# Optimization experiments

Measured on AMD Instinct MI355X. Metric: run time of the kernel, lower is better.

The kernel has to match this reference:

```python
import jax, jax.numpy as jnp
import numpy as np

TOTAL = 409600   # flattened number of (id, rating) pairs across the batch
BATCH = 4096     # number of ragged segments (samples)
VOCAB = 1000000  # sum(field_dims)
DIM = 64         # embed_dim


def setup_inputs() -> dict:
    key = jax.random.key(0)
    k1, k2, k3, k4 = jax.random.split(key, 4)
    ids = jax.random.randint(k1, (TOTAL,), 0, VOCAB, dtype=jnp.int32)
    ratings = jax.random.uniform(k2, (TOTAL,), dtype=jnp.float32)
    segment_ids = jnp.sort(jax.random.randint(k3, (TOTAL,), 0, BATCH, dtype=jnp.int32))
    # Embedding table (xavier_uniform in the original; scale is irrelevant for correctness)
    table = jax.random.normal(k4, (VOCAB, DIM), dtype=jnp.float32) * 0.01
    return {"ids": ids, "ratings": ratings, "segment_ids": segment_ids, "table": table}


def reference(ids, ratings, segment_ids, table):
    # gather rows, scale by ratings, segment-sum over ragged per-sample groups
    emb = table[ids] * ratings[:, None]                      # [TOTAL, DIM]
    out = jax.ops.segment_sum(emb, segment_ids, num_segments=BATCH)  # [BATCH, DIM]
    return out
```

## Files before the change

kernel.cpp:

```cpp
#include <hip/hip_runtime.h>


#define TOTAL 409600
#define BATCH 4096
#define DIM   64
#define WAVES_PER_BLOCK 4

__global__ __launch_bounds__(256) void features_embedding_kernel(
    const int*   __restrict__ ids,
    const float* __restrict__ ratings,
    const int*   __restrict__ seg,
    const float* __restrict__ table,
    float*       __restrict__ out)
{
    const int wave = threadIdx.x >> 6;
    const int lane = threadIdx.x & 63;
    const int b    = blockIdx.x * WAVES_PER_BLOCK + wave;
    if (b >= BATCH) return;

    int lo = 0, hi = TOTAL;
    while (lo < hi) {
        int mid = (lo + hi) >> 1;
        if (seg[mid] < b) lo = mid + 1; else hi = mid;
    }
    int start = lo;
    hi = TOTAL;
    while (lo < hi) {
        int mid = (lo + hi) >> 1;
        if (seg[mid] < b + 1) lo = mid + 1; else hi = mid;
    }
    int end = lo;

    start = __builtin_amdgcn_readfirstlane(start);
    end   = __builtin_amdgcn_readfirstlane(end);

    float acc = 0.0f;
    int r = start;
    constexpr int U = 8;
    for (; r + U <= end; r += U) {
        int   id[U];
        float rt[U];
        #pragma unroll
        for (int u = 0; u < U; ++u) {
            id[u] = ids[r + u];
            rt[u] = ratings[r + u];
        }
        float v[U];
        #pragma unroll
        for (int u = 0; u < U; ++u)
            v[u] = table[(size_t)id[u] * DIM + lane];
        #pragma unroll
        for (int u = 0; u < U; ++u)
            acc = fmaf(v[u], rt[u], acc);
    }
    for (; r < end; ++r)
        acc = fmaf(table[(size_t)ids[r] * DIM + lane], ratings[r], acc);

    out[(size_t)b * DIM + lane] = acc;
}

extern "C" void kernel_launch(void* const* d_in, const int* in_sizes, int n_in,
                              void* d_out, int out_size, void* d_ws, size_t ws_size,
                              hipStream_t stream) {
    const int*   ids     = (const int*)  d_in[0];
    const float* ratings = (const float*)d_in[1];
    const int*   seg     = (const int*)  d_in[2];
    const float* table   = (const float*)d_in[3];
    float*       out     = (float*)      d_out;

    dim3 grid(BATCH / WAVES_PER_BLOCK);
    dim3 block(256);
    features_embedding_kernel<<<grid, block, 0, stream>>>(ids, ratings, seg, table, out);
}
```

Measured before the change: 326.5 us.

## Precompute segment offsets and gather rows with float4 across lane groups

Adds a pre-pass kernel that writes segment start offsets into the workspace, replacing the per-wave binary searches over the segment array. The main kernel now splits each wave into four 16-lane groups, and each group loads a whole 256-byte row as float4s, so four rows are in flight per wave instruction. A cross-group shuffle reduction follows before the store. The cost is an extra kernel launch and fewer independent rows per lane in the unrolled loop (4 instead of 8).

New measurement: 316.7 us. 3.0% less time.

```diff
diff --git a/kernel.cpp b/kernel.cpp
--- a/kernel.cpp
+++ b/kernel.cpp
@@ -4,59 +4,84 @@
 #define TOTAL 409600
 #define BATCH 4096
 #define DIM   64
-#define WAVES_PER_BLOCK 4
 
-__global__ __launch_bounds__(256) void features_embedding_kernel(
+__global__ __launch_bounds__(256) void seg_offsets_kernel(
+    const int* __restrict__ seg, int* __restrict__ offsets)
+{
+    int i = blockIdx.x * blockDim.x + threadIdx.x;
+    if (i >= TOTAL) return;
+    int cur  = seg[i];
+    int prev = (i == 0) ? -1 : seg[i - 1];
+    for (int b = prev + 1; b <= cur; ++b) offsets[b] = i;
+    if (i == TOTAL - 1) {
+        for (int b = cur + 1; b <= BATCH; ++b) offsets[b] = TOTAL;
+    }
+}
+
+__global__ __launch_bounds__(256) void embed_bag_kernel(
     const int*   __restrict__ ids,
     const float* __restrict__ ratings,
-    const int*   __restrict__ seg,
+    const int*   __restrict__ offsets,
     const float* __restrict__ table,
     float*       __restrict__ out)
 {
     const int wave = threadIdx.x >> 6;
     const int lane = threadIdx.x & 63;
-    const int b    = blockIdx.x * WAVES_PER_BLOCK + wave;
-    if (b >= BATCH) return;
+    const int b    = blockIdx.x * 4 + wave;
+    const int grp  = lane >> 4;
+    const int col  = lane & 15;
 
-    int lo = 0, hi = TOTAL;
-    while (lo < hi) {
-        int mid = (lo + hi) >> 1;
-        if (seg[mid] < b) lo = mid + 1; else hi = mid;
-    }
-    int start = lo;
-    hi = TOTAL;
-    while (lo < hi) {
-        int mid = (lo + hi) >> 1;
-        if (seg[mid] < b + 1) lo = mid + 1; else hi = mid;
-    }
-    int end = lo;
+    const int start = offsets[b];
+    const int end   = offsets[b + 1];
+    const int n     = end - start;
 
-    start = __builtin_amdgcn_readfirstlane(start);
-    end   = __builtin_amdgcn_readfirstlane(end);
+    float4 acc = make_float4(0.f, 0.f, 0.f, 0.f);
 
-    float acc = 0.0f;
-    int r = start;
-    constexpr int U = 8;
-    for (; r + U <= end; r += U) {
+    constexpr int U = 4;
+    const int full = start + (n / (4 * U)) * (4 * U);
+
+    for (int base = start; base < full; base += 4 * U) {
         int   id[U];
         float rt[U];
         #pragma unroll
         for (int u = 0; u < U; ++u) {
-            id[u] = ids[r + u];
-            rt[u] = ratings[r + u];
+            int row = base + 4 * u + grp;
+            id[u] = ids[row];
+            rt[u] = ratings[row];
         }
-        float v[U];
         #pragma unroll
-        for (int u = 0; u < U; ++u)
-            v[u] = table[(size_t)id[u] * DIM + lane];
-        #pragma unroll
-        for (int u = 0; u < U; ++u)
-            acc = fmaf(v[u], rt[u], acc);
+        for (int u = 0; u < U; ++u) {
+            const float4 v = ((const float4*)(table + (size_t)id[u] * DIM))[col];
+            acc.x = fmaf(v.x, rt[u], acc.x);
+            acc.y = fmaf(v.y, rt[u], acc.y);
+            acc.z = fmaf(v.z, rt[u], acc.z);
+            acc.w = fmaf(v.w, rt[u], acc.w);
+        }
     }
-    for (; r < end; ++r)
-        acc = fmaf(table[(size_t)ids[r] * DIM + lane], ratings[r], acc);
 
-    out[(size_t)b * DIM + lane] = acc;
+    for (int base = full; base < end; base += 4) {
+        int row = base + grp;
+        if (row < end) {
+            int   id = ids[row];
+            float rt = ratings[row];
+            const float4 v = ((const float4*)(table + (size_t)id * DIM))[col];
+            acc.x = fmaf(v.x, rt, acc.x);
+            acc.y = fmaf(v.y, rt, acc.y);
+            acc.z = fmaf(v.z, rt, acc.z);
+            acc.w = fmaf(v.w, rt, acc.w);
+        }
+    }
+
+    #pragma unroll
+    for (int m = 16; m <= 32; m <<= 1) {
+        acc.x += __shfl_xor(acc.x, m);
+        acc.y += __shfl_xor(acc.y, m);
+        acc.z += __shfl_xor(acc.z, m);
+        acc.w += __shfl_xor(acc.w, m);
+    }
+    if (grp == 0) {
+        ((float4*)(out + (size_t)b * DIM))[col] = acc;
+    }
 }
 
 extern "C" void kernel_launch(void* const* d_in, const int* in_sizes, int n_in,
@@ -67,8 +92,8 @@
     const int*   seg     = (const int*)  d_in[2];
     const float* table   = (const float*)d_in[3];
     float*       out     = (float*)      d_out;
+    int*         offsets = (int*)        d_ws;
 
-    dim3 grid(BATCH / WAVES_PER_BLOCK);
-    dim3 block(256);
-    features_embedding_kernel<<<grid, block, 0, stream>>>(ids, ratings, seg, table, out);
+    seg_offsets_kernel<<<(TOTAL + 255) / 256, 256, 0, stream>>>(seg, offsets);
+    embed_bag_kernel<<<BATCH / 4, 256, 0, stream>>>(ids, ratings, offsets, table, out);
 }
```
